# Optimization experiments

Hardware: AMD Instinct MI355X
Metric: run time of the kernel (lower is better)

Reference implementation:

```python
import jax, jax.numpy as jnp
import numpy as np

R = 8  # rnn_radius
C = 64  # channels


def _shift(x, dh, dw):
    # out[b, h, w, c] = x[b, h - dh, w - dw, c], zero padded (matches SAME conv with a single masked tap)
    B, H, W, Cc = x.shape
    x = jnp.pad(x, ((0, 0), (max(dh, 0), max(-dh, 0)), (max(dw, 0), max(-dw, 0)), (0, 0)))
    return x[:, max(-dh, 0):max(-dh, 0) + H, max(-dw, 0):max(-dw, 0) + W, :]


def _direction(x, W, dh, dw):
    # recurrent: t = relu(shift(t) @ W); acc = x + sum_t over R steps
    def step(carry, _):
        t, acc = carry
        t = jax.nn.relu(jnp.einsum('bhwc,cd->bhwd', _shift(t, dh, dw), W))
        return (t, acc + t), None
    (_, acc), _ = jax.lax.scan(step, (x, x), None, length=R)
    return acc


def setup_inputs() -> dict:
    key = jax.random.key(0)
    kx, kl, kr, ku, kd = jax.random.split(key, 5)
    x = jax.random.normal(kx, (8, 192, 192, C), dtype=jnp.float32)
    # masked kernels reduce to a single CxC channel-mix matrix per direction
    # (keras 'random_normal' initializer: stddev 0.05)
    W_left = jax.random.normal(kl, (C, C), dtype=jnp.float32) * 0.05
    W_right = jax.random.normal(kr, (C, C), dtype=jnp.float32) * 0.05
    W_up = jax.random.normal(ku, (C, C), dtype=jnp.float32) * 0.05
    W_down = jax.random.normal(kd, (C, C), dtype=jnp.float32) * 0.05
    return {"x": x, "W_left": W_left, "W_right": W_right, "W_up": W_up, "W_down": W_down}


def reference(x, W_left, W_right, W_up, W_down):
    # kernel_switch tap positions: left -> out[w]=in[w-1]; right -> out[w]=in[w+1];
    # up -> out[h]=in[h-1]; down -> out[h]=in[h+1]
    outs = [
        _direction(x, W_left, 0, 1),
        _direction(x, W_right, 0, -1),
        _direction(x, W_up, 1, 0),
        _direction(x, W_down, -1, 0),
    ]
    return jnp.concatenate(outs, axis=3)
```

## Files before the change

### kernel.cpp

```cpp
#include <hip/hip_runtime.h>
#include <hip/hip_bf16.h>


#define HD 192
#define CH 64
#define RSTEPS 8
#define TSTRIDE 72
#define SLOTS 193
#define STG_STRIDE 68

typedef __attribute__((ext_vector_type(8))) short short8v;
typedef __attribute__((ext_vector_type(4))) float float4v;

static __device__ __forceinline__ short f2bf_rne(float f) {
    unsigned u = __float_as_uint(f);
    u += 0x7FFFu + ((u >> 16) & 1u);
    return (short)(u >> 16);
}

__global__ __launch_bounds__(256) void spatial_rnn_kernel(
    const float* __restrict__ x,
    const float* __restrict__ Wl,
    const float* __restrict__ Wr,
    const float* __restrict__ Wu,
    const float* __restrict__ Wd,
    float* __restrict__ out)
{
    __shared__ __align__(16) short smem_s[2 * SLOTS * TSTRIDE];
    short* tb0 = smem_s;
    short* tb1 = smem_s + SLOTS * TSTRIDE;
    float* stg = (float*)smem_s;

    const int tid  = threadIdx.x;
    const int dir  = blockIdx.y;
    const int line = blockIdx.x;
    const int b    = line / HD;
    const int rc   = line - b * HD;

    const float* Wp = (dir == 0) ? Wl : (dir == 1) ? Wr : (dir == 2) ? Wu : Wd;

    int xbase, xstride, obase, ostride;
    if (dir == 0) {
        xbase   = (b * HD + rc) * HD * CH;
        xstride = CH;
        obase   = (b * HD + rc) * HD * 256;
        ostride = 256;
    } else if (dir == 1) {
        xbase   = ((b * HD + rc) * HD + (HD - 1)) * CH;
        xstride = -CH;
        obase   = ((b * HD + rc) * HD + (HD - 1)) * 256 + 64;
        ostride = -256;
    } else if (dir == 2) {
        xbase   = b * HD * HD * CH + rc * CH;
        xstride = HD * CH;
        obase   = b * HD * HD * 256 + rc * 256 + 128;
        ostride = HD * 256;
    } else {
        xbase   = ((b * HD + (HD - 1)) * HD + rc) * CH;
        xstride = -HD * CH;
        obase   = ((b * HD + (HD - 1)) * HD + rc) * 256 + 192;
        ostride = -HD * 256;
    }

    for (int q = tid; q < HD * 16; q += 256) {
        int p  = q >> 4;
        int c4 = (q & 15) << 2;
        const float4 v = *(const float4*)(x + xbase + p * xstride + c4);
        short4 s;
        s.x = f2bf_rne(v.x); s.y = f2bf_rne(v.y);
        s.z = f2bf_rne(v.z); s.w = f2bf_rne(v.w);
        *(short4*)(tb0 + (p + 1) * TSTRIDE + c4) = s;
    }
    if (tid < TSTRIDE) { tb0[tid] = 0; tb1[tid] = 0; }

    const int lane = tid & 63;
    const int wv   = tid >> 6;
    const int q4   = lane >> 4;
    const int l16  = lane & 15;

    short8v Af[2][4];
    #pragma unroll
    for (int kc = 0; kc < 2; ++kc)
        #pragma unroll
        for (int dt = 0; dt < 4; ++dt)
            #pragma unroll
            for (int j = 0; j < 8; ++j)
                Af[kc][dt][j] = f2bf_rne(Wp[(kc * 32 + q4 * 8 + j) * CH + dt * 16 + l16]);

    float4v acc[3][4];
    #pragma unroll
    for (int i = 0; i < 3; ++i)
        #pragma unroll
        for (int dt = 0; dt < 4; ++dt)
            acc[i][dt] = (float4v){0.f, 0.f, 0.f, 0.f};

    __syncthreads();

    for (int k = 0; k < RSTEPS; ++k) {
        const short* cur = (k & 1) ? tb1 : tb0;
        short*       nxt = (k & 1) ? tb0 : tb1;
        #pragma unroll
        for (int i = 0; i < 3; ++i) {
            const int pb   = (wv + i * 4) * 16;
            const int slot = pb + l16;
            short8v B0 = *(const short8v*)(cur + slot * TSTRIDE + q4 * 8);
            short8v B1 = *(const short8v*)(cur + slot * TSTRIDE + 32 + q4 * 8);
            #pragma unroll
            for (int dt = 0; dt < 4; ++dt) {
                float4v d = {0.f, 0.f, 0.f, 0.f};
                d = __builtin_amdgcn_mfma_f32_16x16x32_bf16(Af[0][dt], B0, d, 0, 0, 0);
                d = __builtin_amdgcn_mfma_f32_16x16x32_bf16(Af[1][dt], B1, d, 0, 0, 0);
                float v0 = fmaxf(d[0], 0.f);
                float v1 = fmaxf(d[1], 0.f);
                float v2 = fmaxf(d[2], 0.f);
                float v3 = fmaxf(d[3], 0.f);
                acc[i][dt][0] += v0; acc[i][dt][1] += v1;
                acc[i][dt][2] += v2; acc[i][dt][3] += v3;
                if (k < RSTEPS - 1) {
                    __hip_bfloat162 h01 = __float22bfloat162_rn(make_float2(v0, v1));
                    __hip_bfloat162 h23 = __float22bfloat162_rn(make_float2(v2, v3));
                    uint2 wpk;
                    __builtin_memcpy(&wpk.x, &h01, 4);
                    __builtin_memcpy(&wpk.y, &h23, 4);
                    *(uint2*)(nxt + (pb + l16 + 1) * TSTRIDE + dt * 16 + q4 * 4) = wpk;
                }
            }
        }
        __syncthreads();
    }

    #pragma unroll
    for (int i = 0; i < 3; ++i) {
        const int pb = (wv + i * 4) * 16;
        #pragma unroll
        for (int dt = 0; dt < 4; ++dt) {
            *(float4v*)(stg + (pb + l16) * STG_STRIDE + dt * 16 + q4 * 4) = acc[i][dt];
        }
    }
    __syncthreads();

    for (int q = tid; q < HD * 16; q += 256) {
        int p  = q >> 4;
        int c4 = (q & 15) << 2;
        const float4  xv = *(const float4*)(x + xbase + p * xstride + c4);
        const float4v sv = *(const float4v*)(stg + p * STG_STRIDE + c4);
        float4 o;
        o.x = xv.x + sv[0]; o.y = xv.y + sv[1];
        o.z = xv.z + sv[2]; o.w = xv.w + sv[3];
        *(float4*)(out + obase + p * ostride + c4) = o;
    }
}

extern "C" void kernel_launch(void* const* d_in, const int* in_sizes, int n_in,
                              void* d_out, int out_size, void* d_ws, size_t ws_size,
                              hipStream_t stream) {
    const float* x  = (const float*)d_in[0];
    const float* Wl = (const float*)d_in[1];
    const float* Wr = (const float*)d_in[2];
    const float* Wu = (const float*)d_in[3];
    const float* Wd = (const float*)d_in[4];
    float* outp = (float*)d_out;
    dim3 grid(8 * HD, 4);
    spatial_rnn_kernel<<<grid, 256, 0, stream>>>(x, Wl, Wr, Wu, Wd, outp);
}
```

Before: 519.0 us.

## Single-buffer recurrent state in LDS and stage output in chunks for occupancy

Replaces the double-buffered bf16 state in shared memory with one buffer. New values are held in registers, and an extra barrier separates the reads from the writes back. The final accumulator staging is done in three 64-position chunks so it fits in the smaller LDS allocation. Launch bounds request 4 blocks per CU. Halving LDS per block (about 55KB to about 28KB) is meant to raise occupancy, at the cost of more barriers and more register pressure.

```diff
diff --git a/kernel.cpp b/kernel.cpp
--- a/kernel.cpp
+++ b/kernel.cpp
@@ -18,7 +18,7 @@
     return (short)(u >> 16);
 }
 
-__global__ __launch_bounds__(256) void spatial_rnn_kernel(
+__global__ __launch_bounds__(256, 4) void spatial_rnn_kernel(
     const float* __restrict__ x,
     const float* __restrict__ Wl,
     const float* __restrict__ Wr,
@@ -26,9 +26,7 @@
     const float* __restrict__ Wd,
     float* __restrict__ out)
 {
-    __shared__ __align__(16) short smem_s[2 * SLOTS * TSTRIDE];
-    short* tb0 = smem_s;
-    short* tb1 = smem_s + SLOTS * TSTRIDE;
+    __shared__ __align__(16) short smem_s[SLOTS * TSTRIDE];
     float* stg = (float*)smem_s;
 
     const int tid  = threadIdx.x;
@@ -69,9 +67,9 @@
         short4 s;
         s.x = f2bf_rne(v.x); s.y = f2bf_rne(v.y);
         s.z = f2bf_rne(v.z); s.w = f2bf_rne(v.w);
-        *(short4*)(tb0 + (p + 1) * TSTRIDE + c4) = s;
+        *(short4*)(smem_s + (p + 1) * TSTRIDE + c4) = s;
     }
-    if (tid < TSTRIDE) { tb0[tid] = 0; tb1[tid] = 0; }
+    if (tid < TSTRIDE) smem_s[tid] = 0;
 
     const int lane = tid & 63;
     const int wv   = tid >> 6;
@@ -94,26 +92,31 @@
         for (int dt = 0; dt < 4; ++dt)
             acc[i][dt] = (float4v){0.f, 0.f, 0.f, 0.f};
 
+    int rdbase[3], wrbase[3];
+    #pragma unroll
+    for (int i = 0; i < 3; ++i) {
+        const int slot = (wv + i * 4) * 16 + l16;
+        rdbase[i] = (slot * TSTRIDE + q4 * 8) * 2;
+        wrbase[i] = ((slot + 1) * TSTRIDE + q4 * 4) * 2;
+    }
+
     __syncthreads();
 
+    uint2 tnew[3][4];
     for (int k = 0; k < RSTEPS; ++k) {
-        const short* cur = (k & 1) ? tb1 : tb0;
-        short*       nxt = (k & 1) ? tb0 : tb1;
         #pragma unroll
         for (int i = 0; i < 3; ++i) {
-            const int pb   = (wv + i * 4) * 16;
-            const int slot = pb + l16;
-            short8v B0 = *(const short8v*)(cur + slot * TSTRIDE + q4 * 8);
-            short8v B1 = *(const short8v*)(cur + slot * TSTRIDE + 32 + q4 * 8);
+            const short8v B0 = *(const short8v*)((const char*)smem_s + rdbase[i]);
+            const short8v B1 = *(const short8v*)((const char*)smem_s + rdbase[i] + 64);
             #pragma unroll
             for (int dt = 0; dt < 4; ++dt) {
                 float4v d = {0.f, 0.f, 0.f, 0.f};
                 d = __builtin_amdgcn_mfma_f32_16x16x32_bf16(Af[0][dt], B0, d, 0, 0, 0);
                 d = __builtin_amdgcn_mfma_f32_16x16x32_bf16(Af[1][dt], B1, d, 0, 0, 0);
-                float v0 = fmaxf(d[0], 0.f);
-                float v1 = fmaxf(d[1], 0.f);
-                float v2 = fmaxf(d[2], 0.f);
-                float v3 = fmaxf(d[3], 0.f);
+                const float v0 = fmaxf(d[0], 0.f);
+                const float v1 = fmaxf(d[1], 0.f);
+                const float v2 = fmaxf(d[2], 0.f);
+                const float v3 = fmaxf(d[3], 0.f);
                 acc[i][dt][0] += v0; acc[i][dt][1] += v1;
                 acc[i][dt][2] += v2; acc[i][dt][3] += v3;
                 if (k < RSTEPS - 1) {
@@ -122,32 +125,40 @@
                     uint2 wpk;
                     __builtin_memcpy(&wpk.x, &h01, 4);
                     __builtin_memcpy(&wpk.y, &h23, 4);
-                    *(uint2*)(nxt + (pb + l16 + 1) * TSTRIDE + dt * 16 + q4 * 4) = wpk;
+                    tnew[i][dt] = wpk;
                 }
             }
         }
+        if (k == RSTEPS - 1) break;
+        __syncthreads();
+        #pragma unroll
+        for (int i = 0; i < 3; ++i)
+            #pragma unroll
+            for (int dt = 0; dt < 4; ++dt)
+                *(uint2*)((char*)smem_s + wrbase[i] + dt * 32) = tnew[i][dt];
         __syncthreads();
     }
 
     #pragma unroll
     for (int i = 0; i < 3; ++i) {
-        const int pb = (wv + i * 4) * 16;
+        __syncthreads();
         #pragma unroll
-        for (int dt = 0; dt < 4; ++dt) {
-            *(float4v*)(stg + (pb + l16) * STG_STRIDE + dt * 16 + q4 * 4) = acc[i][dt];
+        for (int dt = 0; dt < 4; ++dt)
+            *(float4v*)(stg + (wv * 16 + l16) * STG_STRIDE + dt * 16 + q4 * 4) = acc[i][dt];
+        __syncthreads();
+        #pragma unroll
+        for (int r = 0; r < 4; ++r) {
+            const int q  = tid + r * 256;
+            const int pl = q >> 4;
+            const int c4 = (q & 15) << 2;
+            const int p  = i * 64 + pl;
+            const float4  xv = *(const float4*)(x + xbase + p * xstride + c4);
+            const float4v sv = *(const float4v*)(stg + pl * STG_STRIDE + c4);
+            float4 o;
+            o.x = xv.x + sv[0]; o.y = xv.y + sv[1];
+            o.z = xv.z + sv[2]; o.w = xv.w + sv[3];
+            *(float4*)(out + obase + p * ostride + c4) = o;
         }
-    }
-    __syncthreads();
-
-    for (int q = tid; q < HD * 16; q += 256) {
-        int p  = q >> 4;
-        int c4 = (q & 15) << 2;
-        const float4  xv = *(const float4*)(x + xbase + p * xstride + c4);
-        const float4v sv = *(const float4v*)(stg + p * STG_STRIDE + c4);
-        float4 o;
-        o.x = xv.x + sv[0]; o.y = xv.y + sv[1];
-        o.z = xv.z + sv[2]; o.w = xv.w + sv[3];
-        *(float4*)(out + obase + p * ostride + c4) = o;
     }
 }
 
```

New measurement: 1.251 ms. +141.0%, slower.
